# Optimization experiments

Measured on AMD Instinct MI355X. Metric: run time of the kernel, lower is better.

The kernel has to match this reference:

```python
import jax, jax.numpy as jnp
import numpy as np

N_ENT = 100000
N_REL = 500
D_IN = 128
D_OUT = 128
E_HALF = 1000000  # edges per direction; edge_index has 2*E_HALF columns
BN_EPS = 1e-5


def ccorr(a, b):
    # circular correlation: irfft(conj(rfft(a)) * rfft(b))
    d = a.shape[-1]
    return jnp.fft.irfft(jnp.conj(jnp.fft.rfft(a, axis=-1)) * jnp.fft.rfft(b, axis=-1), n=d, axis=-1)


def setup_inputs() -> dict:
    key = jax.random.key(0)
    ks = jax.random.split(key, 12)
    inv = 1.0 / np.sqrt(D_IN)
    inp = {
        "x": jax.random.normal(ks[0], (N_ENT, D_IN), dtype=jnp.float32),
        "rel_embed": jax.random.normal(ks[1], (N_REL, D_IN), dtype=jnp.float32),
        "w_in": jax.random.uniform(ks[2], (D_IN, D_OUT), minval=-inv, maxval=inv, dtype=jnp.float32),
        "w_out": jax.random.uniform(ks[3], (D_IN, D_OUT), minval=-inv, maxval=inv, dtype=jnp.float32),
        "w_loop": jax.random.uniform(ks[4], (D_IN, D_OUT), minval=-inv, maxval=inv, dtype=jnp.float32),
        "w_rel": jax.random.uniform(ks[5], (D_IN, D_OUT), minval=-inv, maxval=inv, dtype=jnp.float32),
        "loop_rel": jax.random.normal(ks[6], (1, D_IN), dtype=jnp.float32),
        "bias": jnp.zeros((D_OUT,), dtype=jnp.float32),
        "bn_weight": jnp.ones((D_OUT,), dtype=jnp.float32),
        "bn_bias": jnp.zeros((D_OUT,), dtype=jnp.float32),
        "edge_index": jax.random.randint(ks[7], (2, 2 * E_HALF), 0, N_ENT, dtype=jnp.int32),
        "edge_type": jax.random.randint(ks[8], (2 * E_HALF,), 0, N_REL, dtype=jnp.int32),
    }
    return inp


def _compute_norm(edge_index, num_ent):
    row, col = edge_index[0], edge_index[1]
    ones = jnp.ones(row.shape, dtype=jnp.float32)
    deg = jax.ops.segment_sum(ones, row, num_segments=num_ent)
    deg_inv = jnp.where(deg > 0, jax.lax.rsqrt(jnp.maximum(deg, 1.0)), 0.0)
    return deg_inv[row] * deg_inv[col]  # [E]


def _propagate(x, edge_index, edge_type, rel_all, weight, norm, num_ent):
    x_j = x[edge_index[0]]              # [E, d_in] gather source nodes
    r = rel_all[edge_type]              # [E, d_in] gather relation embeds
    m = ccorr(x_j, r) @ weight          # [E, d_out]
    if norm is not None:
        m = m * norm[:, None]
    return jax.ops.segment_sum(m, edge_index[1], num_segments=num_ent)


def reference(x, rel_embed, w_in, w_out, w_loop, w_rel, loop_rel, bias, bn_weight, bn_bias, edge_index, edge_type):
    num_ent = x.shape[0]
    rel_all = jnp.concatenate([rel_embed, loop_rel], axis=0)  # [R+1, d_in]
    e = edge_index.shape[1] // 2
    in_idx, out_idx = edge_index[:, :e], edge_index[:, e:]
    in_type, out_type = edge_type[:e], edge_type[e:]

    in_norm = _compute_norm(in_idx, num_ent)
    out_norm = _compute_norm(out_idx, num_ent)

    in_res = _propagate(x, in_idx, in_type, rel_all, w_in, in_norm, num_ent)
    out_res = _propagate(x, out_idx, out_type, rel_all, w_out, out_norm, num_ent)
    # loop edges are (i, i) with relation = last row of rel_all -> identity scatter
    loop_res = ccorr(x, rel_all[-1][None, :]) @ w_loop

    out = (in_res + out_res + loop_res) * (1.0 / 3.0) + bias
    # BatchNorm1d (training-mode batch statistics, biased variance)
    mu = jnp.mean(out, axis=0)
    var = jnp.mean((out - mu) ** 2, axis=0)
    out = (out - mu) * jax.lax.rsqrt(var + BN_EPS) * bn_weight + bn_bias

    rel_out = (rel_all @ w_rel)[:-1]
    return out, rel_out
```

## Files before the change

kernel.cpp:

```cpp
#include <hip/hip_runtime.h>
#include <cmath>

#define N_ENT 100000
#define EHALF 1000000
#define N_REL 500
#define NBUK 196
#define DPB 512
#define SCAP 7680
#define DCAP 6656
#define NSB 512
#define SPAN 1954

#ifndef M_PI
#define M_PI 3.14159265358979323846
#endif

typedef _Float16 f16x8 __attribute__((ext_vector_type(8)));
typedef _Float16 f16x4 __attribute__((ext_vector_type(4)));
typedef _Float16 f16x2 __attribute__((ext_vector_type(2)));
typedef float f32x4 __attribute__((ext_vector_type(4)));

union H16 { unsigned short u; _Float16 h; };
union HU32 { unsigned u; f16x2 h; };

__global__ void k_tabs(float* __restrict__ Ftab, float* __restrict__ Gtab,
                       _Float16* __restrict__ FtabT) {
  int i = blockIdx.x * 256 + threadIdx.x;
  if (i >= 128 * 128) return;
  int n = i >> 7, s = i & 127;
  float fv, gv;
  if (s == 0) { fv = 1.f; gv = 1.f / 384.f; }
  else if (s == 1) { float sg = (n & 1) ? -1.f : 1.f; fv = sg; gv = sg / 384.f; }
  else {
    int f = s >> 1;
    double ang = 2.0 * M_PI * (double)((f * n) & 127) / 128.0;
    if (!(s & 1)) { double c = cos(ang); fv = (float)c; gv = (float)(c * (2.0 / 384.0)); }
    else { double sv = sin(ang); fv = (float)(-sv); gv = (float)(-sv * (2.0 / 384.0)); }
  }
  Ftab[n * 128 + s] = fv;
  Gtab[s * 128 + n] = gv;
  FtabT[s * 128 + n] = (_Float16)fv;
}

__global__ void k_dftrel(const float* __restrict__ rel, const float* __restrict__ looprel,
                         const float* __restrict__ Ftab, float* __restrict__ Rf,
                         _Float16* __restrict__ RfL) {
  __shared__ float sv[128];
  int r = blockIdx.x, s = threadIdx.x;
  const float* row = (r < N_REL) ? rel + (size_t)r * 128 : looprel;
  float acc = 0.f;
  for (int n = 0; n < 128; ++n) acc += row[n] * Ftab[n * 128 + s];
  Rf[(size_t)r * 128 + s] = acc;
  sv[s] = acc;
  __syncthreads();
  if (s < 64) {
    f16x4 o;
    if (s == 0) {
      o = (f16x4){(_Float16)sv[0], (_Float16)0.f, (_Float16)0.f, (_Float16)sv[1]};
    } else {
      float rx = sv[2 * s], ry = sv[2 * s + 1];
      o = (f16x4){(_Float16)rx, (_Float16)ry, (_Float16)ry, (_Float16)(-rx)};
    }
    ((f16x4*)RfL)[(size_t)r * 64 + s] = o;
  }
}

__global__ void k_wt(const float* __restrict__ W, const float* __restrict__ Rfl,
                     _Float16* __restrict__ WT) {
  int i = blockIdx.x * 256 + threadIdx.x;
  if (i >= 384 * 128) return;
  int k = i >> 7, c = i & 127;
  float val;
  if (k < 256) {
    val = W[i];
  } else {
    int kk = k - 256;
    if (kk == 0)      val = Rfl[0] * W[i];
    else if (kk == 1) val = Rfl[1] * W[i];
    else {
      int f = kk >> 1;
      float rr = Rfl[2 * f], ri = Rfl[2 * f + 1];
      float a = W[(256 + 2 * f) * 128 + c];
      float b = W[(256 + 2 * f + 1) * 128 + c];
      val = (kk & 1) ? (ri * a - rr * b) : (rr * a + ri * b);
    }
  }
  WT[(size_t)c * 384 + k] = (_Float16)val;
}

__device__ void gemm128_body(const float* __restrict__ A, int lda,
                             const float* __restrict__ B,
                             float* __restrict__ C, int ldc,
                             int M, int K, int m0) {
  __shared__ float As[64][64];
  __shared__ float Bs[64][128];
  const int t = threadIdx.x;
  const int cg = t & 31;
  const int eg = t >> 5;
  float acc[8][4];
#pragma unroll
  for (int i = 0; i < 8; ++i)
#pragma unroll
    for (int j = 0; j < 4; ++j) acc[i][j] = 0.f;

  for (int k0 = 0; k0 < K; k0 += 64) {
#pragma unroll
    for (int p = 0; p < 4; ++p) {
      int idx = t + p * 256;
      int r = idx >> 4, c4 = idx & 15;
      int gr = m0 + r;
      float4 v = make_float4(0.f, 0.f, 0.f, 0.f);
      if (gr < M) v = *(const float4*)(A + (size_t)gr * lda + k0 + c4 * 4);
      *(float4*)&As[r][c4 * 4] = v;
    }
#pragma unroll
    for (int p = 0; p < 8; ++p) {
      int idx = t + p * 256;
      int r = idx >> 5, c4 = idx & 31;
      float4 v = *(const float4*)(B + (size_t)(k0 + r) * 128 + c4 * 4);
      *(float4*)&Bs[r][c4 * 4] = v;
    }
    __syncthreads();
#pragma unroll
    for (int k = 0; k < 64; ++k) {
      float4 bv = *(float4*)&Bs[k][cg * 4];
#pragma unroll
      for (int i = 0; i < 8; ++i) {
        float av = As[eg * 8 + i][k];
        acc[i][0] += av * bv.x; acc[i][1] += av * bv.y;
        acc[i][2] += av * bv.z; acc[i][3] += av * bv.w;
      }
    }
    __syncthreads();
  }
#pragma unroll
  for (int i = 0; i < 8; ++i) {
    int gr = m0 + eg * 8 + i;
    if (gr < M) {
      float4 v = make_float4(acc[i][0], acc[i][1], acc[i][2], acc[i][3]);
      *(float4*)(C + (size_t)gr * ldc + cg * 4) = v;
    }
  }
}

__global__ __launch_bounds__(256) void gemm128(
    const float* __restrict__ A, int lda, const float* __restrict__ B,
    float* __restrict__ C, int ldc, int M, int K) {
  gemm128_body(A, lda, B, C, ldc, M, K, blockIdx.x * 64);
}

__global__ __launch_bounds__(256) void k_wprep(
    const float* __restrict__ Gtab, const float* __restrict__ w0,
    const float* __restrict__ w1, const float* __restrict__ w2,
    float* __restrict__ Wstack) {
  int which = blockIdx.x >> 1;
  const float* B = (which == 0) ? w0 : ((which == 1) ? w1 : w2);
  gemm128_body(Gtab, 128, B, Wstack + which * 128 * 128, 128, 128, 128,
               (blockIdx.x & 1) * 64);
}

__device__ inline f16x8 loadAfrag(const _Float16* A, size_t off) {
  return *(const f16x8*)(A + off);
}
__device__ inline f16x8 loadAfrag(const float* A, size_t off) {
  float4 u = *(const float4*)(A + off);
  float4 v = *(const float4*)(A + off + 4);
  return (f16x8){(_Float16)u.x, (_Float16)u.y, (_Float16)u.z, (_Float16)u.w,
                 (_Float16)v.x, (_Float16)v.y, (_Float16)v.z, (_Float16)v.w};
}

template<int K, int KS, int MODE, typename AT>
__global__ __launch_bounds__(256) void mgemm(
    const AT* __restrict__ A, int lda,
    const _Float16* __restrict__ BT,
    _Float16* __restrict__ C, int ldc, int M,
    const float* __restrict__ bias, float* __restrict__ bnAcc) {
  __shared__ __align__(16) char lds[128 * KS * 2 + 4096];
  const int t = threadIdx.x;
  const int l = t & 63, w = t >> 6;
  const int col0 = l & 15, rg = l >> 4;
  const int rowbase = blockIdx.x * 256 + w * 64;
  const int sw = (col0 & 7) << 4;

  f32x4 acc[4][8];
  f32x4 zz = {0.f, 0.f, 0.f, 0.f};
#pragma unroll
  for (int a = 0; a < 4; ++a)
#pragma unroll
    for (int n = 0; n < 8; ++n) acc[a][n] = zz;

  for (int ks0 = 0; ks0 < K; ks0 += KS) {
    __syncthreads();
    const int CH = KS / 8;
    for (int u = t; u < 128 * CH; u += 256) {
      int col = u / CH, kc = u % CH;
      f16x8 vch = *(const f16x8*)(BT + (size_t)col * K + ks0 + kc * 8);
      *(f16x8*)(lds + col * (KS * 2) + ((kc * 16) ^ ((col & 7) << 4))) = vch;
    }
    __syncthreads();
#pragma unroll
    for (int ks = 0; ks < KS / 32; ++ks) {
      int kb = ks0 + ks * 32 + rg * 8;
      f16x8 af[4];
#pragma unroll
      for (int a = 0; a < 4; ++a) {
        int rb = rowbase + a * 16;
        if (rb < M) af[a] = loadAfrag(A, (size_t)(rb + col0) * lda + kb);
        else af[a] = (f16x8){0, 0, 0, 0, 0, 0, 0, 0};
      }
      int kc = ks * 4 + rg;
#pragma unroll
      for (int n = 0; n < 8; ++n) {
        f16x8 bf = *(const f16x8*)(lds + (n * 16 + col0) * (KS * 2) + ((kc * 16) ^ sw));
#pragma unroll
        for (int a = 0; a < 4; ++a)
          acc[a][n] = __builtin_amdgcn_mfma_f32_16x16x32_f16(af[a], bf, acc[a][n], 0, 0, 0);
      }
    }
  }

  if (MODE == 1) {
#pragma unroll
    for (int a = 0; a < 4; ++a) {
      int rb = rowbase + a * 16;
      if (rb >= M) continue;
#pragma unroll
      for (int r = 0; r < 4; ++r) {
        int row = rb + rg * 4 + r;
#pragma unroll
        for (int n = 0; n < 8; ++n) {
          int col = n * 16 + col0;
          C[(size_t)row * ldc + col] = (_Float16)acc[a][n][r];
        }
      }
    }
  } else {
    float sacc[8], qacc[8];
#pragma unroll
    for (int n = 0; n < 8; ++n) { sacc[n] = 0.f; qacc[n] = 0.f; }
#pragma unroll
    for (int a = 0; a < 4; ++a) {
      int rb = rowbase + a * 16;
      if (rb >= M) continue;
#pragma unroll
      for (int n = 0; n < 8; ++n) {
        int col = n * 16 + col0;
        float bi = bias[col];
#pragma unroll
        for (int r = 0; r < 4; ++r) {
          float val = acc[a][n][r] + bi;
          C[(size_t)(rb + rg * 4 + r) * ldc + col] = (_Float16)val;
          sacc[n] += val; qacc[n] += val * val;
        }
      }
    }
    __syncthreads();
    float* Sb = (float*)lds;
    float* Qb = Sb + 512;
#pragma unroll
    for (int n = 0; n < 8; ++n) {
      float s = sacc[n], q = qacc[n];
      s += __shfl_xor(s, 16); s += __shfl_xor(s, 32);
      q += __shfl_xor(q, 16); q += __shfl_xor(q, 32);
      if (rg == 0) { Sb[w * 128 + n * 16 + col0] = s; Qb[w * 128 + n * 16 + col0] = q; }
    }
    __syncthreads();
    if (t < 128) {
      float s = Sb[t] + Sb[128 + t] + Sb[256 + t] + Sb[384 + t];
      float q = Qb[t] + Qb[128 + t] + Qb[256 + t] + Qb[384 + t];
      atomicAdd(&bnAcc[t], s);
      atomicAdd(&bnAcc[128 + t], q);
    }
  }
}

__global__ __launch_bounds__(256) void k_split(
    const int* __restrict__ ei, const int* __restrict__ et,
    int* __restrict__ gcur,
    unsigned* __restrict__ recSI, unsigned* __restrict__ recSO,
    uint2* __restrict__ recDI, uint2* __restrict__ recDO) {
  __shared__ int bcnt[NBUK], cnt2[NBUK], base[NBUK], nn[NBUK];
  const int t = threadIdx.x;
  const int ph = blockIdx.x >> 9;
  const int blk = blockIdx.x & 511;
  const int st = blk * SPAN;
  const int en = min(st + SPAN, EHALF);

  if (t < NBUK) { bcnt[t] = 0; cnt2[t] = 0; }
  __syncthreads();

  if (ph < 2) {
    const int* key = ei + (ph ? EHALF : 0);
    int* gc = gcur + ph * NBUK;
    unsigned* rec = ph ? recSO : recSI;
    unsigned rr[8]; int bb[8];
#pragma unroll
    for (int j = 0; j < 8; ++j) {
      int e = st + j * 256 + t;
      bb[j] = -1;
      if (e < en) {
        int s = key[e];
        rr[j] = (unsigned)(s & 511) | 0x80000000u;
        bb[j] = s >> 9;
        atomicAdd(&bcnt[bb[j]], 1);
      }
    }
    __syncthreads();
    if (t < NBUK) {
      int n = bcnt[t]; nn[t] = n;
      base[t] = n ? (t * SCAP + atomicAdd(&gc[t], (n + 7) & ~7)) : 0;
    }
    __syncthreads();
#pragma unroll
    for (int j = 0; j < 8; ++j) {
      if (bb[j] >= 0) {
        int p = atomicAdd(&cnt2[bb[j]], 1);
        rec[(size_t)base[bb[j]] + p] = rr[j];
      }
    }
    __syncthreads();
    if (t < NBUK) {
      int n = nn[t];
      if (n & 7) {
        int pe = (n + 7) & ~7;
        for (int k = n; k < pe; ++k) rec[(size_t)base[t] + k] = 0u;
      }
    }
  } else {
    const int dir = ph - 2;
    const int* srcA = ei + (dir ? EHALF : 0);
    const int* dstA = ei + (dir ? 3 * EHALF : 2 * EHALF);
    const int* typA = et + (dir ? EHALF : 0);
    int* gc = gcur + (2 + dir) * NBUK;
    uint2* rec = dir ? recDO : recDI;
    unsigned w0[8], w1[8]; int bb[8];
#pragma unroll
    for (int j = 0; j < 8; ++j) {
      int e = st + j * 256 + t;
      bb[j] = -1;
      if (e < en) {
        int s = srcA[e], d = dstA[e], ty = typA[e];
        w0[j] = (unsigned)s | ((unsigned)ty << 17);
        w1[j] = (unsigned)(d & 511) | 0x80000000u;
        bb[j] = d >> 9;
        atomicAdd(&bcnt[bb[j]], 1);
      }
    }
    __syncthreads();
    if (t < NBUK) {
      int n = bcnt[t]; nn[t] = n;
      base[t] = n ? (t * DCAP + atomicAdd(&gc[t], (n + 3) & ~3)) : 0;
    }
    __syncthreads();
#pragma unroll
    for (int j = 0; j < 8; ++j) {
      if (bb[j] >= 0) {
        int p = atomicAdd(&cnt2[bb[j]], 1);
        rec[(size_t)base[bb[j]] + p] = make_uint2(w0[j], w1[j]);
      }
    }
    __syncthreads();
    if (t < NBUK) {
      int n = nn[t];
      if (n & 3) {
        int pe = (n + 3) & ~3;
        for (int k = n; k < pe; ++k) rec[(size_t)base[t] + k] = make_uint2(0u, 0u);
      }
    }
  }
}

__global__ __launch_bounds__(512) void k_dhist(
    const unsigned* __restrict__ recI, const int* __restrict__ gI,
    float* __restrict__ dinvIn,
    const unsigned* __restrict__ recO, const int* __restrict__ gO,
    float* __restrict__ dinvOut) {
  int b = blockIdx.x % NBUK;
  int dir = blockIdx.x / NBUK;
  const unsigned* rec = dir ? recO : recI;
  const int gs = b * SCAP;
  const int ge = gs + (dir ? gO : gI)[b];
  float* dinv = dir ? dinvOut : dinvIn;
  __shared__ int h[DPB];
  int t = threadIdx.x;
  h[t] = 0;
  __syncthreads();
  for (int i = gs + t; i < ge; i += 512) {
    unsigned r = rec[i];
    if (r >> 31) atomicAdd(&h[r & 511], 1);
  }
  __syncthreads();
  int ent = b * 512 + t;
  if (ent < N_ENT) {
    int d = h[t];
    dinv[ent] = (d > 0) ? rsqrtf((float)d) : 0.f;
  }
}

__global__ __launch_bounds__(512) void k_fsort(
    const uint2* __restrict__ recDI, const int* __restrict__ gDI,
    uint2* __restrict__ csrIn, int2* __restrict__ beI,
    const uint2* __restrict__ recDO, const int* __restrict__ gDO,
    uint2* __restrict__ csrOut, int2* __restrict__ beO,
    const float* __restrict__ dinvIn, const float* __restrict__ dinvOut) {
  int b = blockIdx.x % NBUK;
  int dir = blockIdx.x / NBUK;
  const uint2* rec = dir ? recDO : recDI;
  const int gs = b * DCAP;
  const int ge = gs + (dir ? gDO : gDI)[b];
  const float* dinv = dir ? dinvOut : dinvIn;
  uint2* csr = dir ? csrOut : csrIn;
  int2* be = dir ? beO : beI;
  __shared__ int h[DPB], sc[DPB], c2[DPB];
  __shared__ float dl[DPB];
  __shared__ int totv;
  int t = threadIdx.x;
  int ent = b * 512 + t;
  h[t] = 0; c2[t] = 0;
  dl[t] = (ent < N_ENT) ? dinv[ent] : 0.f;
  __syncthreads();
  for (int i = gs + t; i < ge; i += 512) {
    uint2 r = rec[i];
    if (r.y >> 31) atomicAdd(&h[r.y & 511], 1);
  }
  __syncthreads();
  sc[t] = h[t];
  __syncthreads();
  for (int o = 1; o < 512; o <<= 1) {
    int a = (t >= o) ? sc[t - o] : 0;
    __syncthreads();
    sc[t] += a;
    __syncthreads();
  }
  int excl = sc[t] - h[t];
  if (t == 511) totv = sc[511];
  if (ent < N_ENT) be[ent] = make_int2(gs + excl, gs + excl + h[t]);
  __syncthreads();
  sc[t] = excl;
  __syncthreads();
  if (t < 8) csr[(size_t)gs + totv + t] = make_uint2(0u, 0u);
  for (int i = gs + t; i < ge; i += 512) {
    uint2 r = rec[i];
    if (r.y >> 31) {
      int d = r.y & 511;
      unsigned src = r.x & 0x1FFFFu;
      float nm = dinv[src] * dl[d];
      H16 cv; cv.h = (_Float16)nm;
      int p = atomicAdd(&c2[d], 1);
      csr[(size_t)gs + sc[d] + p] =
          make_uint2((src * 3u) << 8,
                     (r.x >> 17) | ((unsigned)cv.u << 16));
    }
  }
}

__device__ inline float dot2f(f16x2 a, f16x2 b, float c) {
#if __has_builtin(__builtin_amdgcn_fdot2)
  return __builtin_amdgcn_fdot2(a, b, c, false);
#else
  return fmaf((float)a[0], (float)b[0], fmaf((float)a[1], (float)b[1], c));
#endif
}

__device__ inline void b4load(const uint2* __restrict__ csr, int base,
                              const char* __restrict__ Xb, const char* __restrict__ Rb,
                              unsigned lxc, unsigned lr,
                              uint2 q[4], f16x2 xv[4], f16x4 rv[4]) {
// ... 48 lines not shown
  while (nbi > 0) {
    uint2 qa[4]; f16x2 xa[4]; f16x4 ra[4];
    b4load(csrIn, i, Xb, Rb, lxc, lr, qa, xa, ra);
    b4math(qa, i, ie, xa, ra, aix, aiy);
    i += 4; --nbi;
  }
  while (nbo > 0) {
    uint2 qb[4]; f16x2 xb[4]; f16x4 rb[4];
    b4load(csrOut, o, Xb, Rb, lxc, lr, qb, xb, rb);
    b4math(qb, o, oe, xb, rb, aox, aoy);
    o += 4; --nbo;
  }

  *(f16x2*)((char*)Abuf + (size_t)v * 768 + 4u * l) = (f16x2){(_Float16)aix, (_Float16)aiy};
  *(f16x2*)((char*)Abuf + (size_t)v * 768 + 256 + 4u * l) = (f16x2){(_Float16)aox, (_Float16)aoy};
}

__global__ void k_norm(const _Float16* __restrict__ tmp, float* __restrict__ out,
                       const float* __restrict__ bnAcc, const float* __restrict__ bnw,
                       const float* __restrict__ bnb) {
  __shared__ float ss[256];
  int t = threadIdx.x;
  if (t < 128) {
    float mu = bnAcc[t] * (1.f / (float)N_ENT);
    float var = bnAcc[128 + t] * (1.f / (float)N_ENT) - mu * mu;
    float sc = bnw[t] * rsqrtf(var + 1e-5f);
    ss[t] = sc; ss[128 + t] = bnb[t] - mu * sc;
  }
  __syncthreads();
  int i = blockIdx.x * 256 + t;
  f16x8 v = ((const f16x8*)tmp)[i];
  int cb = (i & 15) * 8;
  float4 o0, o1;
  o0.x = (float)v[0] * ss[cb]     + ss[128 + cb];
  o0.y = (float)v[1] * ss[cb + 1] + ss[129 + cb];
  o0.z = (float)v[2] * ss[cb + 2] + ss[130 + cb];
  o0.w = (float)v[3] * ss[cb + 3] + ss[131 + cb];
  o1.x = (float)v[4] * ss[cb + 4] + ss[132 + cb];
  o1.y = (float)v[5] * ss[cb + 5] + ss[133 + cb];
  o1.z = (float)v[6] * ss[cb + 6] + ss[134 + cb];
  o1.w = (float)v[7] * ss[cb + 7] + ss[135 + cb];
  ((float4*)out)[2 * i] = o0;
  ((float4*)out)[2 * i + 1] = o1;
}

extern "C" void kernel_launch(void* const* d_in, const int* in_sizes, int n_in,
                              void* d_out, int out_size, void* d_ws, size_t ws_size,
                              hipStream_t stream) {
  const float* x       = (const float*)d_in[0];
  const float* rel     = (const float*)d_in[1];
  const float* w_in    = (const float*)d_in[2];
  const float* w_out   = (const float*)d_in[3];
  const float* w_loop  = (const float*)d_in[4];
  const float* w_rel   = (const float*)d_in[5];
  const float* looprel = (const float*)d_in[6];
  const float* bias    = (const float*)d_in[7];
  const float* bnw     = (const float*)d_in[8];
  const float* bnb     = (const float*)d_in[9];
// ... 19 lines not shown
  float* dinvIn   = (float*)alloc(N_ENT * 4);
  float* dinvOut  = (float*)alloc(N_ENT * 4);
  int*   gcur     = (int*)alloc(4 * NBUK * 4);
  int2*  beI      = (int2*)alloc((size_t)N_ENT * 8);
  int2*  beO      = (int2*)alloc((size_t)N_ENT * 8);
  unsigned* recSI = (unsigned*)alloc((size_t)NBUK * SCAP * 4);
  unsigned* recSO = (unsigned*)alloc((size_t)NBUK * SCAP * 4);
  uint2* recDI    = (uint2*)alloc((size_t)NBUK * DCAP * 8);
  uint2* recDO    = (uint2*)alloc((size_t)NBUK * DCAP * 8);
  uint2* csrIn    = (uint2*)alloc((size_t)NBUK * DCAP * 8);
  uint2* csrOut   = (uint2*)alloc((size_t)NBUK * DCAP * 8);
  float* bnAcc    = (float*)alloc(256 * 4);

  int* gSI = gcur;
  int* gSO = gcur + NBUK;

  hipMemsetAsync(gcur, 0, 4 * NBUK * 4, stream);
  hipMemsetAsync(bnAcc, 0, 256 * 4, stream);

  k_tabs<<<64, 256, 0, stream>>>(Ftab, Gtab, FtabT);
  k_dftrel<<<501, 128, 0, stream>>>(rel, looprel, Ftab, Rf, RfL);
  k_wprep<<<6, 256, 0, stream>>>(Gtab, w_in, w_out, w_loop, Wstack);
  k_wt<<<192, 256, 0, stream>>>(Wstack, Rf + 500 * 128, WT);

  mgemm<128, 128, 1, float><<<(N_ENT + 255) / 256, 256, 0, stream>>>(
      x, 128, FtabT, Abuf + 256, 384, N_ENT, nullptr, nullptr);

  k_split<<<4 * NSB, 256, 0, stream>>>(ei, et, gcur, recSI, recSO, recDI, recDO);
  k_dhist<<<2 * NBUK, 512, 0, stream>>>(recSI, gSI, dinvIn, recSO, gSO, dinvOut);
  k_fsort<<<2 * NBUK, 512, 0, stream>>>(recDI, gcur + 2 * NBUK, csrIn, beI,
                                        recDO, gcur + 3 * NBUK, csrOut, beO,
                                        dinvIn, dinvOut);

  k_agg<<<N_ENT / 4, 256, 0, stream>>>(Abuf, RfL, csrIn, beI, csrOut, beO);

  mgemm<384, 192, 2, _Float16><<<(N_ENT + 255) / 256, 256, 0, stream>>>(
      Abuf, 384, WT, tmpC, 128, N_ENT, bias, bnAcc);
  k_norm<<<(N_ENT * 128 / 8) / 256, 256, 0, stream>>>(tmpC, out, bnAcc, bnw, bnb);

  gemm128<<<(N_REL + 63) / 64, 256, 0, stream>>>(rel, 128, w_rel, out + (size_t)N_ENT * 128, 128, N_REL, 128);
}
```

Baseline: 309.8 us.

## Fuse independent small kernels into combined launches to cut launch count

Merges independent stages into multi-role kernels that dispatch on block index. The x DFT GEMM, edge split and relation DFT share one launch, weight prep shares one with degree histogram, and the weight transpose shares one with the CSR sort. The relation GEMM shares a launch with the final normalization. The two memsets move into the table-building kernel. This cuts launch count and serialization gaps between small kernels. The cost is shared LDS sized for the largest role and larger per-launch register footprints, which may lower occupancy for some roles.

```diff
diff --git a/kernel.cpp b/kernel.cpp
--- a/kernel.cpp
+++ b/kernel.cpp
@@ -10,6 +10,7 @@
 #define DCAP 6656
 #define NSB 512
 #define SPAN 1954
+#define XFB 391
 
 #ifndef M_PI
 #define M_PI 3.14159265358979323846
@@ -24,7 +25,12 @@
 union HU32 { unsigned u; f16x2 h; };
 
 __global__ void k_tabs(float* __restrict__ Ftab, float* __restrict__ Gtab,
-                       _Float16* __restrict__ FtabT) {
+                       _Float16* __restrict__ FtabT,
+                       int* __restrict__ gcur, float* __restrict__ bnAcc) {
+  if (blockIdx.x == 0) {
+    for (int j = threadIdx.x; j < 4 * NBUK; j += 256) gcur[j] = 0;
+    bnAcc[threadIdx.x] = 0.f;
+  }
   int i = blockIdx.x * 256 + threadIdx.x;
   if (i >= 128 * 128) return;
   int n = i >> 7, s = i & 127;
@@ -42,32 +48,396 @@
   FtabT[s * 128 + n] = (_Float16)fv;
 }
 
-__global__ void k_dftrel(const float* __restrict__ rel, const float* __restrict__ looprel,
-                         const float* __restrict__ Ftab, float* __restrict__ Rf,
-                         _Float16* __restrict__ RfL) {
-  __shared__ float sv[128];
-  int r = blockIdx.x, s = threadIdx.x;
-  const float* row = (r < N_REL) ? rel + (size_t)r * 128 : looprel;
-  float acc = 0.f;
-  for (int n = 0; n < 128; ++n) acc += row[n] * Ftab[n * 128 + s];
-  Rf[(size_t)r * 128 + s] = acc;
-  sv[s] = acc;
-  __syncthreads();
-  if (s < 64) {
+__device__ void gemm128_body(char* smem, const float* __restrict__ A, int lda,
+                             const float* __restrict__ B,
+                             float* __restrict__ C, int ldc,
+                             int M, int K, int m0) {
+  float (*As)[64] = (float(*)[64])smem;
+  float (*Bs)[128] = (float(*)[128])(smem + 64 * 64 * 4);
+  const int t = threadIdx.x;
+  const int cg = t & 31;
+  const int eg = t >> 5;
+  float acc[8][4];
+#pragma unroll
+  for (int i = 0; i < 8; ++i)
+#pragma unroll
+    for (int j = 0; j < 4; ++j) acc[i][j] = 0.f;
+
+  for (int k0 = 0; k0 < K; k0 += 64) {
+#pragma unroll
+    for (int p = 0; p < 4; ++p) {
+      int idx = t + p * 256;
+      int r = idx >> 4, c4 = idx & 15;
+      int gr = m0 + r;
+      float4 v = make_float4(0.f, 0.f, 0.f, 0.f);
+      if (gr < M) v = *(const float4*)(A + (size_t)gr * lda + k0 + c4 * 4);
+      *(float4*)&As[r][c4 * 4] = v;
+    }
+#pragma unroll
+    for (int p = 0; p < 8; ++p) {
+      int idx = t + p * 256;
+      int r = idx >> 5, c4 = idx & 31;
+      float4 v = *(const float4*)(B + (size_t)(k0 + r) * 128 + c4 * 4);
+      *(float4*)&Bs[r][c4 * 4] = v;
+    }
+    __syncthreads();
+#pragma unroll
+    for (int k = 0; k < 64; ++k) {
+      float4 bv = *(float4*)&Bs[k][cg * 4];
+#pragma unroll
+      for (int i = 0; i < 8; ++i) {
+        float av = As[eg * 8 + i][k];
+        acc[i][0] += av * bv.x; acc[i][1] += av * bv.y;
+        acc[i][2] += av * bv.z; acc[i][3] += av * bv.w;
+      }
+    }
+    __syncthreads();
+  }
+#pragma unroll
+  for (int i = 0; i < 8; ++i) {
+    int gr = m0 + eg * 8 + i;
+    if (gr < M) {
+      float4 v = make_float4(acc[i][0], acc[i][1], acc[i][2], acc[i][3]);
+      *(float4*)(C + (size_t)gr * ldc + cg * 4) = v;
+    }
+  }
+}
+
+__device__ inline f16x8 loadAfrag(const _Float16* A, size_t off) {
+  return *(const f16x8*)(A + off);
+}
+__device__ inline f16x8 loadAfrag(const float* A, size_t off) {
+  float4 u = *(const float4*)(A + off);
+  float4 v = *(const float4*)(A + off + 4);
+  return (f16x8){(_Float16)u.x, (_Float16)u.y, (_Float16)u.z, (_Float16)u.w,
+                 (_Float16)v.x, (_Float16)v.y, (_Float16)v.z, (_Float16)v.w};
+}
+
+template<int K, int KS, int MODE, typename AT>
+__device__ void mgemm_body(char* lds, int bid,
+                           const AT* __restrict__ A, int lda,
+                           const _Float16* __restrict__ BT,
+                           _Float16* __restrict__ C, int ldc, int M,
+                           const float* __restrict__ bias, float* __restrict__ bnAcc) {
+  const int t = threadIdx.x;
+  const int l = t & 63, w = t >> 6;
+  const int col0 = l & 15, rg = l >> 4;
+  const int rowbase = bid * 256 + w * 64;
+  const int sw = (col0 & 7) << 4;
+
+  f32x4 acc[4][8];
+  f32x4 zz = {0.f, 0.f, 0.f, 0.f};
+#pragma unroll
+  for (int a = 0; a < 4; ++a)
+#pragma unroll
+    for (int n = 0; n < 8; ++n) acc[a][n] = zz;
+
+  for (int ks0 = 0; ks0 < K; ks0 += KS) {
+    __syncthreads();
+    const int CH = KS / 8;
+    for (int u = t; u < 128 * CH; u += 256) {
+      int col = u / CH, kc = u % CH;
+      f16x8 vch = *(const f16x8*)(BT + (size_t)col * K + ks0 + kc * 8);
+      *(f16x8*)(lds + col * (KS * 2) + ((kc * 16) ^ ((col & 7) << 4))) = vch;
+    }
+    __syncthreads();
+#pragma unroll
+    for (int ks = 0; ks < KS / 32; ++ks) {
+      int kb = ks0 + ks * 32 + rg * 8;
+      f16x8 af[4];
+#pragma unroll
+      for (int a = 0; a < 4; ++a) {
+        int rb = rowbase + a * 16;
+        if (rb < M) af[a] = loadAfrag(A, (size_t)(rb + col0) * lda + kb);
+        else af[a] = (f16x8){0, 0, 0, 0, 0, 0, 0, 0};
+      }
+      int kc = ks * 4 + rg;
+#pragma unroll
+      for (int n = 0; n < 8; ++n) {
+        f16x8 bf = *(const f16x8*)(lds + (n * 16 + col0) * (KS * 2) + ((kc * 16) ^ sw));
+#pragma unroll
+        for (int a = 0; a < 4; ++a)
+          acc[a][n] = __builtin_amdgcn_mfma_f32_16x16x32_f16(af[a], bf, acc[a][n], 0, 0, 0);
+      }
+    }
+  }
+
+  if (MODE == 1) {
+#pragma unroll
+    for (int a = 0; a < 4; ++a) {
+      int rb = rowbase + a * 16;
+      if (rb >= M) continue;
+#pragma unroll
+      for (int r = 0; r < 4; ++r) {
+        int row = rb + rg * 4 + r;
+#pragma unroll
+        for (int n = 0; n < 8; ++n) {
+          int col = n * 16 + col0;
+          C[(size_t)row * ldc + col] = (_Float16)acc[a][n][r];
+        }
+      }
+    }
+  } else {
+    float sacc[8], qacc[8];
+#pragma unroll
+    for (int n = 0; n < 8; ++n) { sacc[n] = 0.f; qacc[n] = 0.f; }
+#pragma unroll
+    for (int a = 0; a < 4; ++a) {
+      int rb = rowbase + a * 16;
+      if (rb >= M) continue;
+#pragma unroll
+      for (int n = 0; n < 8; ++n) {
+        int col = n * 16 + col0;
+        float bi = bias[col];
+#pragma unroll
+        for (int r = 0; r < 4; ++r) {
+          float val = acc[a][n][r] + bi;
+          C[(size_t)(rb + rg * 4 + r) * ldc + col] = (_Float16)val;
+          sacc[n] += val; qacc[n] += val * val;
+        }
+      }
+    }
+    __syncthreads();
+    float* Sb = (float*)lds;
+    float* Qb = Sb + 512;
+#pragma unroll
+    for (int n = 0; n < 8; ++n) {
+      float s = sacc[n], q = qacc[n];
+      s += __shfl_xor(s, 16); s += __shfl_xor(s, 32);
+      q += __shfl_xor(q, 16); q += __shfl_xor(q, 32);
+      if (rg == 0) { Sb[w * 128 + n * 16 + col0] = s; Qb[w * 128 + n * 16 + col0] = q; }
+    }
+    __syncthreads();
+    if (t < 128) {
+      float s = Sb[t] + Sb[128 + t] + Sb[256 + t] + Sb[384 + t];
+      float q = Qb[t] + Qb[128 + t] + Qb[256 + t] + Qb[384 + t];
+      atomicAdd(&bnAcc[t], s);
+      atomicAdd(&bnAcc[128 + t], q);
+    }
+  }
+}
+
+__device__ void split_body(char* smem, int bid,
+                           const int* __restrict__ ei, const int* __restrict__ et,
+                           int* __restrict__ gcur,
+                           unsigned* __restrict__ recSI, unsigned* __restrict__ recSO,
+                           uint2* __restrict__ recDI, uint2* __restrict__ recDO) {
+  int* bcnt = (int*)smem;
+  int* cnt2 = bcnt + NBUK;
+  int* base = cnt2 + NBUK;
+  int* nn   = base + NBUK;
+  const int t = threadIdx.x;
+  const int ph = bid >> 9;
+  const int blk = bid & 511;
+  const int st = blk * SPAN;
+  const int en = min(st + SPAN, EHALF);
+
+  if (t < NBUK) { bcnt[t] = 0; cnt2[t] = 0; }
+  __syncthreads();
+
+  if (ph < 2) {
+    const int* key = ei + (ph ? EHALF : 0);
+    int* gc = gcur + ph * NBUK;
+    unsigned* rec = ph ? recSO : recSI;
+    unsigned rr[8]; int bb[8];
+#pragma unroll
+    for (int j = 0; j < 8; ++j) {
+      int e = st + j * 256 + t;
+      bb[j] = -1;
+      if (e < en) {
+        int s = key[e];
+        rr[j] = (unsigned)(s & 511) | 0x80000000u;
+        bb[j] = s >> 9;
+        atomicAdd(&bcnt[bb[j]], 1);
+      }
+    }
+    __syncthreads();
+    if (t < NBUK) {
+      int n = bcnt[t]; nn[t] = n;
+      base[t] = n ? (t * SCAP + atomicAdd(&gc[t], (n + 7) & ~7)) : 0;
+    }
+    __syncthreads();
+#pragma unroll
+    for (int j = 0; j < 8; ++j) {
+      if (bb[j] >= 0) {
+        int p = atomicAdd(&cnt2[bb[j]], 1);
+        rec[(size_t)base[bb[j]] + p] = rr[j];
+      }
+    }
+    __syncthreads();
+    if (t < NBUK) {
+      int n = nn[t];
+      if (n & 7) {
+        int pe = (n + 7) & ~7;
+        for (int k = n; k < pe; ++k) rec[(size_t)base[t] + k] = 0u;
+      }
+    }
+  } else {
+    const int dir = ph - 2;
+    const int* srcA = ei + (dir ? EHALF : 0);
+    const int* dstA = ei + (dir ? 3 * EHALF : 2 * EHALF);
+    const int* typA = et + (dir ? EHALF : 0);
+    int* gc = gcur + (2 + dir) * NBUK;
+    uint2* rec = dir ? recDO : recDI;
+    unsigned w0[8], w1[8]; int bb[8];
+#pragma unroll
+    for (int j = 0; j < 8; ++j) {
+      int e = st + j * 256 + t;
+      bb[j] = -1;
+      if (e < en) {
+        int s = srcA[e], d = dstA[e], ty = typA[e];
+        w0[j] = (unsigned)s | ((unsigned)ty << 17);
+        w1[j] = (unsigned)(d & 511) | 0x80000000u;
+        bb[j] = d >> 9;
+        atomicAdd(&bcnt[bb[j]], 1);
+      }
+    }
+    __syncthreads();
+    if (t < NBUK) {
+      int n = bcnt[t]; nn[t] = n;
+      base[t] = n ? (t * DCAP + atomicAdd(&gc[t], (n + 3) & ~3)) : 0;
+    }
+    __syncthreads();
+#pragma unroll
+    for (int j = 0; j < 8; ++j) {
+      if (bb[j] >= 0) {
+        int p = atomicAdd(&cnt2[bb[j]], 1);
+        rec[(size_t)base[bb[j]] + p] = make_uint2(w0[j], w1[j]);
+      }
+    }
+    __syncthreads();
+    if (t < NBUK) {
+      int n = nn[t];
+      if (n & 3) {
+        int pe = (n + 3) & ~3;
+        for (int k = n; k < pe; ++k) rec[(size_t)base[t] + k] = make_uint2(0u, 0u);
+      }
+    }
+  }
+}
+
+__device__ void dftrel_body(char* smem, int blk,
+                            const float* __restrict__ rel, const float* __restrict__ looprel,
+                            const float* __restrict__ Ftab, float* __restrict__ Rf,
+                            _Float16* __restrict__ RfL) {
+  float* sv = (float*)smem;
+  int t = threadIdx.x;
+  int r = blk * 2 + (t >> 7);
+  int s = t & 127;
+  if (r < 501) {
+    const float* row = (r < N_REL) ? rel + (size_t)r * 128 : looprel;
+    float acc = 0.f;
+    for (int n = 0; n < 128; ++n) acc += row[n] * Ftab[n * 128 + s];
+    Rf[(size_t)r * 128 + s] = acc;
+    sv[t] = acc;
+  }
+  __syncthreads();
+  if (r < 501 && s < 64) {
+    int bse = t & 128;
     f16x4 o;
     if (s == 0) {
-      o = (f16x4){(_Float16)sv[0], (_Float16)0.f, (_Float16)0.f, (_Float16)sv[1]};
+      o = (f16x4){(_Float16)sv[bse], (_Float16)0.f, (_Float16)0.f, (_Float16)sv[bse + 1]};
     } else {
-      float rx = sv[2 * s], ry = sv[2 * s + 1];
+      float rx = sv[bse + 2 * s], ry = sv[bse + 2 * s + 1];
       o = (f16x4){(_Float16)rx, (_Float16)ry, (_Float16)ry, (_Float16)(-rx)};
     }
     ((f16x4*)RfL)[(size_t)r * 64 + s] = o;
   }
 }
 
-__global__ void k_wt(const float* __restrict__ W, const float* __restrict__ Rfl,
-                     _Float16* __restrict__ WT) {
-  int i = blockIdx.x * 256 + threadIdx.x;
+__device__ void dhist_body(char* smem, int bid,
+                           const unsigned* __restrict__ recI, const int* __restrict__ gI,
+                           float* __restrict__ dinvIn,
+                           const unsigned* __restrict__ recO, const int* __restrict__ gO,
+                           float* __restrict__ dinvOut) {
+  int b = bid % NBUK;
+  int dir = bid / NBUK;
+  const unsigned* rec = dir ? recO : recI;
+  const int gs = b * SCAP;
+  const int ge = gs + (dir ? gO : gI)[b];
+  float* dinv = dir ? dinvOut : dinvIn;
+  int* h = (int*)smem;
+  int t = threadIdx.x;
+  h[t] = 0; h[t + 256] = 0;
+  __syncthreads();
+  for (int i = gs + t; i < ge; i += 256) {
+    unsigned r = rec[i];
+    if (r >> 31) atomicAdd(&h[r & 511], 1);
+  }
+  __syncthreads();
+#pragma unroll
+  for (int j = 0; j < 2; ++j) {
+    int bin = t + j * 256;
+    int ent = b * 512 + bin;
+    if (ent < N_ENT) {
+      int d = h[bin];
+      dinv[ent] = (d > 0) ? rsqrtf((float)d) : 0.f;
+    }
+  }
+}
+
+__device__ void fsort_body(char* smem, int bid,
+                           const uint2* __restrict__ recDI, const int* __restrict__ gDI,
+                           uint2* __restrict__ csrIn, int2* __restrict__ beI,
+                           const uint2* __restrict__ recDO, const int* __restrict__ gDO,
+                           uint2* __restrict__ csrOut, int2* __restrict__ beO,
+                           const float* __restrict__ dinvIn, const float* __restrict__ dinvOut) {
+  int b = bid % NBUK;
+  int dir = bid / NBUK;
+  const uint2* rec = dir ? recDO : recDI;
+  const int gs = b * DCAP;
+  const int ge = gs + (dir ? gDO : gDI)[b];
+  const float* dinv = dir ? dinvOut : dinvIn;
+  uint2* csr = dir ? csrOut : csrIn;
+  int2* be = dir ? beO : beI;
+  int* h  = (int*)smem;
+  int* sc = h + 512;
+  int* c2 = sc + 512;
+  float* dl = (float*)(c2 + 512);
+  int* totv = (int*)(dl + 512);
+  int t = threadIdx.x;
+  int ent = b * 512 + t;
+  h[t] = 0; c2[t] = 0;
+  dl[t] = (ent < N_ENT) ? dinv[ent] : 0.f;
+  __syncthreads();
+  for (int i = gs + t; i < ge; i += 512) {
+    uint2 r = rec[i];
+    if (r.y >> 31) atomicAdd(&h[r.y & 511], 1);
+  }
+  __syncthreads();
+  sc[t] = h[t];
+  __syncthreads();
+  for (int o = 1; o < 512; o <<= 1) {
+    int a = (t >= o) ? sc[t - o] : 0;
+    __syncthreads();
+    sc[t] += a;
+    __syncthreads();
+  }
+  int excl = sc[t] - h[t];
+  if (t == 511) *totv = sc[511];
+  if (ent < N_ENT) be[ent] = make_int2(gs + excl, gs + excl + h[t]);
+  __syncthreads();
+  sc[t] = excl;
+  __syncthreads();
+  if (t < 8) csr[(size_t)gs + *totv + t] = make_uint2(0u, 0u);
+  for (int i = gs + t; i < ge; i += 512) {
+    uint2 r = rec[i];
+    if (r.y >> 31) {
+      int d = r.y & 511;
+      unsigned src = r.x & 0x1FFFFu;
+      float nm = dinv[src] * dl[d];
+      H16 cv; cv.h = (_Float16)nm;
+      int p = atomicAdd(&c2[d], 1);
+      csr[(size_t)gs + sc[d] + p] =
+          make_uint2((src * 3u) << 8,
+                     (r.x >> 17) | ((unsigned)cv.u << 16));
+    }
+  }
+}
+
+__device__ void wt_body(int wb, const float* __restrict__ W, const float* __restrict__ Rfl,
+                        _Float16* __restrict__ WT) {
+  int i = wb * 512 + threadIdx.x;
   if (i >= 384 * 128) return;
   int k = i >> 7, c = i & 127;
   float val;
@@ -88,369 +458,103 @@
   WT[(size_t)c * 384 + k] = (_Float16)val;
 }
 
-__device__ void gemm128_body(const float* __restrict__ A, int lda,
-                             const float* __restrict__ B,
-                             float* __restrict__ C, int ldc,
-                             int M, int K, int m0) {
-  __shared__ float As[64][64];
-  __shared__ float Bs[64][128];
-  const int t = threadIdx.x;
-  const int cg = t & 31;
-  const int eg = t >> 5;
-  float acc[8][4];
-#pragma unroll
-  for (int i = 0; i < 8; ++i)
-#pragma unroll
-    for (int j = 0; j < 4; ++j) acc[i][j] = 0.f;
-
-  for (int k0 = 0; k0 < K; k0 += 64) {
-#pragma unroll
-    for (int p = 0; p < 4; ++p) {
-      int idx = t + p * 256;
-      int r = idx >> 4, c4 = idx & 15;
-      int gr = m0 + r;
-      float4 v = make_float4(0.f, 0.f, 0.f, 0.f);
-      if (gr < M) v = *(const float4*)(A + (size_t)gr * lda + k0 + c4 * 4);
-      *(float4*)&As[r][c4 * 4] = v;
-    }
-#pragma unroll
-    for (int p = 0; p < 8; ++p) {
-      int idx = t + p * 256;
-      int r = idx >> 5, c4 = idx & 31;
-      float4 v = *(const float4*)(B + (size_t)(k0 + r) * 128 + c4 * 4);
-      *(float4*)&Bs[r][c4 * 4] = v;
-    }
-    __syncthreads();
-#pragma unroll
-    for (int k = 0; k < 64; ++k) {
-      float4 bv = *(float4*)&Bs[k][cg * 4];
-#pragma unroll
-      for (int i = 0; i < 8; ++i) {
-        float av = As[eg * 8 + i][k];
-        acc[i][0] += av * bv.x; acc[i][1] += av * bv.y;
-        acc[i][2] += av * bv.z; acc[i][3] += av * bv.w;
-      }
-    }
-    __syncthreads();
-  }
-#pragma unroll
-  for (int i = 0; i < 8; ++i) {
-    int gr = m0 + eg * 8 + i;
-    if (gr < M) {
-      float4 v = make_float4(acc[i][0], acc[i][1], acc[i][2], acc[i][3]);
-      *(float4*)(C + (size_t)gr * ldc + cg * 4) = v;
-    }
-  }
-}
-
-__global__ __launch_bounds__(256) void gemm128(
-    const float* __restrict__ A, int lda, const float* __restrict__ B,
-    float* __restrict__ C, int ldc, int M, int K) {
-  gemm128_body(A, lda, B, C, ldc, M, K, blockIdx.x * 64);
-}
-
-__global__ __launch_bounds__(256) void k_wprep(
+__device__ void norm_body(char* smem, int bid, const _Float16* __restrict__ tmp,
+                          float* __restrict__ out, const float* __restrict__ bnAcc,
+                          const float* __restrict__ bnw, const float* __restrict__ bnb) {
+  float* ss = (float*)smem;
+  int t = threadIdx.x;
+  if (t < 128) {
+    float mu = bnAcc[t] * (1.f / (float)N_ENT);
+    float var = bnAcc[128 + t] * (1.f / (float)N_ENT) - mu * mu;
+    float sc = bnw[t] * rsqrtf(var + 1e-5f);
+    ss[t] = sc; ss[128 + t] = bnb[t] - mu * sc;
+  }
+  __syncthreads();
+  int i = bid * 256 + t;
+  f16x8 v = ((const f16x8*)tmp)[i];
+  int cb = (i & 15) * 8;
+  float4 o0, o1;
+  o0.x = (float)v[0] * ss[cb]     + ss[128 + cb];
+  o0.y = (float)v[1] * ss[cb + 1] + ss[129 + cb];
+  o0.z = (float)v[2] * ss[cb + 2] + ss[130 + cb];
+  o0.w = (float)v[3] * ss[cb + 3] + ss[131 + cb];
+  o1.x = (float)v[4] * ss[cb + 4] + ss[132 + cb];
+  o1.y = (float)v[5] * ss[cb + 5] + ss[133 + cb];
+  o1.z = (float)v[6] * ss[cb + 6] + ss[134 + cb];
+  o1.w = (float)v[7] * ss[cb + 7] + ss[135 + cb];
+  ((float4*)out)[2 * i] = o0;
+  ((float4*)out)[2 * i + 1] = o1;
+}
+
+__global__ __launch_bounds__(256) void k_front(
+    const float* __restrict__ x, const _Float16* __restrict__ FtabT, _Float16* __restrict__ Abuf,
+    const int* __restrict__ ei, const int* __restrict__ et, int* __restrict__ gcur,
+    unsigned* __restrict__ recSI, unsigned* __restrict__ recSO,
+    uint2* __restrict__ recDI, uint2* __restrict__ recDO,
+    const float* __restrict__ rel, const float* __restrict__ looprel,
+    const float* __restrict__ Ftab, float* __restrict__ Rf, _Float16* __restrict__ RfL) {
+  __shared__ __align__(16) char smem[37120];
+  int b = blockIdx.x;
+  if (b < XFB) {
+    mgemm_body<128, 128, 1, float>(smem, b, x, 128, FtabT, Abuf + 256, 384, N_ENT,
+                                   nullptr, nullptr);
+  } else if (b < XFB + 4 * NSB) {
+    split_body(smem, b - XFB, ei, et, gcur, recSI, recSO, recDI, recDO);
+  } else {
+    dftrel_body(smem, b - XFB - 4 * NSB, rel, looprel, Ftab, Rf, RfL);
+  }
+}
+
+__global__ __launch_bounds__(256) void k_mid1(
     const float* __restrict__ Gtab, const float* __restrict__ w0,
-    const float* __restrict__ w1, const float* __restrict__ w2,
-    float* __restrict__ Wstack) {
-  int which = blockIdx.x >> 1;
-  const float* B = (which == 0) ? w0 : ((which == 1) ? w1 : w2);
-  gemm128_body(Gtab, 128, B, Wstack + which * 128 * 128, 128, 128, 128,
-               (blockIdx.x & 1) * 64);
-}
-
-__device__ inline f16x8 loadAfrag(const _Float16* A, size_t off) {
-  return *(const f16x8*)(A + off);
-}
-__device__ inline f16x8 loadAfrag(const float* A, size_t off) {
-  float4 u = *(const float4*)(A + off);
-  float4 v = *(const float4*)(A + off + 4);
-  return (f16x8){(_Float16)u.x, (_Float16)u.y, (_Float16)u.z, (_Float16)u.w,
-                 (_Float16)v.x, (_Float16)v.y, (_Float16)v.z, (_Float16)v.w};
-}
-
-template<int K, int KS, int MODE, typename AT>
-__global__ __launch_bounds__(256) void mgemm(
-    const AT* __restrict__ A, int lda,
-    const _Float16* __restrict__ BT,
-    _Float16* __restrict__ C, int ldc, int M,
-    const float* __restrict__ bias, float* __restrict__ bnAcc) {
-  __shared__ __align__(16) char lds[128 * KS * 2 + 4096];
-  const int t = threadIdx.x;
-  const int l = t & 63, w = t >> 6;
-  const int col0 = l & 15, rg = l >> 4;
-  const int rowbase = blockIdx.x * 256 + w * 64;
-  const int sw = (col0 & 7) << 4;
-
-  f32x4 acc[4][8];
-  f32x4 zz = {0.f, 0.f, 0.f, 0.f};
-#pragma unroll
-  for (int a = 0; a < 4; ++a)
-#pragma unroll
-    for (int n = 0; n < 8; ++n) acc[a][n] = zz;
-
-  for (int ks0 = 0; ks0 < K; ks0 += KS) {
-    __syncthreads();
-    const int CH = KS / 8;
-    for (int u = t; u < 128 * CH; u += 256) {
-      int col = u / CH, kc = u % CH;
-      f16x8 vch = *(const f16x8*)(BT + (size_t)col * K + ks0 + kc * 8);
-      *(f16x8*)(lds + col * (KS * 2) + ((kc * 16) ^ ((col & 7) << 4))) = vch;
-    }
-    __syncthreads();
-#pragma unroll
-    for (int ks = 0; ks < KS / 32; ++ks) {
-      int kb = ks0 + ks * 32 + rg * 8;
-      f16x8 af[4];
-#pragma unroll
-      for (int a = 0; a < 4; ++a) {
-        int rb = rowbase + a * 16;
-        if (rb < M) af[a] = loadAfrag(A, (size_t)(rb + col0) * lda + kb);
-        else af[a] = (f16x8){0, 0, 0, 0, 0, 0, 0, 0};
-      }
-      int kc = ks * 4 + rg;
-#pragma unroll
-      for (int n = 0; n < 8; ++n) {
-        f16x8 bf = *(const f16x8*)(lds + (n * 16 + col0) * (KS * 2) + ((kc * 16) ^ sw));
-#pragma unroll
-        for (int a = 0; a < 4; ++a)
-          acc[a][n] = __builtin_amdgcn_mfma_f32_16x16x32_f16(af[a], bf, acc[a][n], 0, 0, 0);
-      }
-    }
-  }
-
-  if (MODE == 1) {
-#pragma unroll
-    for (int a = 0; a < 4; ++a) {
-      int rb = rowbase + a * 16;
-      if (rb >= M) continue;
-#pragma unroll
-      for (int r = 0; r < 4; ++r) {
-        int row = rb + rg * 4 + r;
-#pragma unroll
-        for (int n = 0; n < 8; ++n) {
-          int col = n * 16 + col0;
-          C[(size_t)row * ldc + col] = (_Float16)acc[a][n][r];
-        }
-      }
-    }
+    const float* __restrict__ w1, const float* __restrict__ w2, float* __restrict__ Wstack,
+    const unsigned* __restrict__ recSI, const int* __restrict__ gSI, float* __restrict__ dinvIn,
+    const unsigned* __restrict__ recSO, const int* __restrict__ gSO, float* __restrict__ dinvOut) {
+  __shared__ __align__(16) char smem[49280];
+  int b = blockIdx.x;
+  if (b < 6) {
+    int which = b >> 1;
+    const float* B = (which == 0) ? w0 : ((which == 1) ? w1 : w2);
+    gemm128_body(smem, Gtab, 128, B, Wstack + which * 128 * 128, 128, 128, 128, (b & 1) * 64);
   } else {
-    float sacc[8], qacc[8];
-#pragma unroll
-    for (int n = 0; n < 8; ++n) { sacc[n] = 0.f; qacc[n] = 0.f; }
-#pragma unroll
-    for (int a = 0; a < 4; ++a) {
-      int rb = rowbase + a * 16;
-      if (rb >= M) continue;
-#pragma unroll
-      for (int n = 0; n < 8; ++n) {
-        int col = n * 16 + col0;
-        float bi = bias[col];
-#pragma unroll
-        for (int r = 0; r < 4; ++r) {
-          float val = acc[a][n][r] + bi;
-          C[(size_t)(rb + rg * 4 + r) * ldc + col] = (_Float16)val;
-          sacc[n] += val; qacc[n] += val * val;
-        }
-      }
-    }
-    __syncthreads();
-    float* Sb = (float*)lds;
-    float* Qb = Sb + 512;
-#pragma unroll
-    for (int n = 0; n < 8; ++n) {
-      float s = sacc[n], q = qacc[n];
-      s += __shfl_xor(s, 16); s += __shfl_xor(s, 32);
-      q += __shfl_xor(q, 16); q += __shfl_xor(q, 32);
-      if (rg == 0) { Sb[w * 128 + n * 16 + col0] = s; Qb[w * 128 + n * 16 + col0] = q; }
-    }
-    __syncthreads();
-    if (t < 128) {
-      float s = Sb[t] + Sb[128 + t] + Sb[256 + t] + Sb[384 + t];
-      float q = Qb[t] + Qb[128 + t] + Qb[256 + t] + Qb[384 + t];
-      atomicAdd(&bnAcc[t], s);
-      atomicAdd(&bnAcc[128 + t], q);
-    }
-  }
-}
-
-__global__ __launch_bounds__(256) void k_split(
-    const int* __restrict__ ei, const int* __restrict__ et,
-    int* __restrict__ gcur,
-    unsigned* __restrict__ recSI, unsigned* __restrict__ recSO,
-    uint2* __restrict__ recDI, uint2* __restrict__ recDO) {
-  __shared__ int bcnt[NBUK], cnt2[NBUK], base[NBUK], nn[NBUK];
-  const int t = threadIdx.x;
-  const int ph = blockIdx.x >> 9;
-  const int blk = blockIdx.x & 511;
-  const int st = blk * SPAN;
-  const int en = min(st + SPAN, EHALF);
-
-  if (t < NBUK) { bcnt[t] = 0; cnt2[t] = 0; }
-  __syncthreads();
-
-  if (ph < 2) {
-    const int* key = ei + (ph ? EHALF : 0);
-    int* gc = gcur + ph * NBUK;
-    unsigned* rec = ph ? recSO : recSI;
-    unsigned rr[8]; int bb[8];
-#pragma unroll
-    for (int j = 0; j < 8; ++j) {
-      int e = st + j * 256 + t;
-      bb[j] = -1;
-      if (e < en) {
-        int s = key[e];
-        rr[j] = (unsigned)(s & 511) | 0x80000000u;
-        bb[j] = s >> 9;
-        atomicAdd(&bcnt[bb[j]], 1);
-      }
-    }
-    __syncthreads();
-    if (t < NBUK) {
-      int n = bcnt[t]; nn[t] = n;
-      base[t] = n ? (t * SCAP + atomicAdd(&gc[t], (n + 7) & ~7)) : 0;
-    }
-    __syncthreads();
-#pragma unroll
-    for (int j = 0; j < 8; ++j) {
-      if (bb[j] >= 0) {
-        int p = atomicAdd(&cnt2[bb[j]], 1);
-        rec[(size_t)base[bb[j]] + p] = rr[j];
-      }
-    }
-    __syncthreads();
-    if (t < NBUK) {
-      int n = nn[t];
-      if (n & 7) {
-        int pe = (n + 7) & ~7;
-        for (int k = n; k < pe; ++k) rec[(size_t)base[t] + k] = 0u;
-      }
-    }
-  } else {
-    const int dir = ph - 2;
-    const int* srcA = ei + (dir ? EHALF : 0);
-    const int* dstA = ei + (dir ? 3 * EHALF : 2 * EHALF);
-    const int* typA = et + (dir ? EHALF : 0);
-    int* gc = gcur + (2 + dir) * NBUK;
-    uint2* rec = dir ? recDO : recDI;
-    unsigned w0[8], w1[8]; int bb[8];
-#pragma unroll
-    for (int j = 0; j < 8; ++j) {
-      int e = st + j * 256 + t;
-      bb[j] = -1;
-      if (e < en) {
-        int s = srcA[e], d = dstA[e], ty = typA[e];
-        w0[j] = (unsigned)s | ((unsigned)ty << 17);
-        w1[j] = (unsigned)(d & 511) | 0x80000000u;
-        bb[j] = d >> 9;
-        atomicAdd(&bcnt[bb[j]], 1);
-      }
-    }
-    __syncthreads();
-    if (t < NBUK) {
-      int n = bcnt[t]; nn[t] = n;
-      base[t] = n ? (t * DCAP + atomicAdd(&gc[t], (n + 3) & ~3)) : 0;
-    }
-    __syncthreads();
-#pragma unroll
-    for (int j = 0; j < 8; ++j) {
-      if (bb[j] >= 0) {
-        int p = atomicAdd(&cnt2[bb[j]], 1);
-        rec[(size_t)base[bb[j]] + p] = make_uint2(w0[j], w1[j]);
-      }
-    }
-    __syncthreads();
-    if (t < NBUK) {
-      int n = nn[t];
-      if (n & 3) {
-        int pe = (n + 3) & ~3;
-        for (int k = n; k < pe; ++k) rec[(size_t)base[t] + k] = make_uint2(0u, 0u);
-      }
-    }
-  }
-}
-
-__global__ __launch_bounds__(512) void k_dhist(
-    const unsigned* __restrict__ recI, const int* __restrict__ gI,
-    float* __restrict__ dinvIn,
-    const unsigned* __restrict__ recO, const int* __restrict__ gO,
-    float* __restrict__ dinvOut) {
-  int b = blockIdx.x % NBUK;
-  int dir = blockIdx.x / NBUK;
-  const unsigned* rec = dir ? recO : recI;
-  const int gs = b * SCAP;
-  const int ge = gs + (dir ? gO : gI)[b];
-  float* dinv = dir ? dinvOut : dinvIn;
-  __shared__ int h[DPB];
-  int t = threadIdx.x;
-  h[t] = 0;
-  __syncthreads();
-  for (int i = gs + t; i < ge; i += 512) {
-    unsigned r = rec[i];
-    if (r >> 31) atomicAdd(&h[r & 511], 1);
-  }
-  __syncthreads();
-  int ent = b * 512 + t;
-  if (ent < N_ENT) {
-    int d = h[t];
-    dinv[ent] = (d > 0) ? rsqrtf((float)d) : 0.f;
-  }
-}
-
-__global__ __launch_bounds__(512) void k_fsort(
+    dhist_body(smem, b - 6, recSI, gSI, dinvIn, recSO, gSO, dinvOut);
+  }
+}
+
+__global__ __launch_bounds__(512) void k_mid2(
     const uint2* __restrict__ recDI, const int* __restrict__ gDI,
     uint2* __restrict__ csrIn, int2* __restrict__ beI,
     const uint2* __restrict__ recDO, const int* __restrict__ gDO,
     uint2* __restrict__ csrOut, int2* __restrict__ beO,
-    const float* __restrict__ dinvIn, const float* __restrict__ dinvOut) {
-  int b = blockIdx.x % NBUK;
-  int dir = blockIdx.x / NBUK;
-  const uint2* rec = dir ? recDO : recDI;
-  const int gs = b * DCAP;
-  const int ge = gs + (dir ? gDO : gDI)[b];
-  const float* dinv = dir ? dinvOut : dinvIn;
-  uint2* csr = dir ? csrOut : csrIn;
-  int2* be = dir ? beO : beI;
-  __shared__ int h[DPB], sc[DPB], c2[DPB];
-  __shared__ float dl[DPB];
-  __shared__ int totv;
-  int t = threadIdx.x;
-  int ent = b * 512 + t;
-  h[t] = 0; c2[t] = 0;
-  dl[t] = (ent < N_ENT) ? dinv[ent] : 0.f;
-  __syncthreads();
-  for (int i = gs + t; i < ge; i += 512) {
-    uint2 r = rec[i];
-    if (r.y >> 31) atomicAdd(&h[r.y & 511], 1);
-  }
-  __syncthreads();
-  sc[t] = h[t];
-  __syncthreads();
-  for (int o = 1; o < 512; o <<= 1) {
-    int a = (t >= o) ? sc[t - o] : 0;
-    __syncthreads();
-    sc[t] += a;
-    __syncthreads();
-  }
-  int excl = sc[t] - h[t];
-  if (t == 511) totv = sc[511];
-  if (ent < N_ENT) be[ent] = make_int2(gs + excl, gs + excl + h[t]);
-  __syncthreads();
-  sc[t] = excl;
-  __syncthreads();
-  if (t < 8) csr[(size_t)gs + totv + t] = make_uint2(0u, 0u);
-  for (int i = gs + t; i < ge; i += 512) {
-    uint2 r = rec[i];
-    if (r.y >> 31) {
-      int d = r.y & 511;
-      unsigned src = r.x & 0x1FFFFu;
-      float nm = dinv[src] * dl[d];
-      H16 cv; cv.h = (_Float16)nm;
-      int p = atomicAdd(&c2[d], 1);
-      csr[(size_t)gs + sc[d] + p] =
-          make_uint2((src * 3u) << 8,
-                     (r.x >> 17) | ((unsigned)cv.u << 16));
-    }
+    const float* __restrict__ dinvIn, const float* __restrict__ dinvOut,
+    const float* __restrict__ Wstack, const float* __restrict__ Rfl, _Float16* __restrict__ WT) {
+  __shared__ __align__(16) char smem[8448];
+  int b = blockIdx.x;
+  if (b < 2 * NBUK) {
+    fsort_body(smem, b, recDI, gDI, csrIn, beI, recDO, gDO, csrOut, beO, dinvIn, dinvOut);
+  } else {
+    wt_body(b - 2 * NBUK, Wstack, Rfl, WT);
+  }
+}
+
+__global__ __launch_bounds__(256) void k_mgemm384(
+    const _Float16* __restrict__ A, const _Float16* __restrict__ BT,
+    _Float16* __restrict__ C, int M,
+    const float* __restrict__ bias, float* __restrict__ bnAcc) {
+  __shared__ __align__(16) char lds[53504];
+  mgemm_body<384, 192, 2, _Float16>(lds, blockIdx.x, A, 384, BT, C, 128, M, bias, bnAcc);
+}
+
+__global__ __launch_bounds__(256) void k_back(
+    const float* __restrict__ rel, const float* __restrict__ w_rel, float* __restrict__ out,
+    const _Float16* __restrict__ tmp, const float* __restrict__ bnAcc,
+    const float* __restrict__ bnw, const float* __restrict__ bnb) {
+  __shared__ __align__(16) char smem[49280];
+  int b = blockIdx.x;
+  if (b < 8) {
+    gemm128_body(smem, rel, 128, w_rel, out + (size_t)N_ENT * 128, 128, N_REL, 128, b * 64);
+  } else {
+    norm_body(smem, b - 8, tmp, out, bnAcc, bnw, bnb);
   }
 }
 
@@ -529,34 +633,6 @@
 
   *(f16x2*)((char*)Abuf + (size_t)v * 768 + 4u * l) = (f16x2){(_Float16)aix, (_Float16)aiy};
   *(f16x2*)((char*)Abuf + (size_t)v * 768 + 256 + 4u * l) = (f16x2){(_Float16)aox, (_Float16)aoy};
-}
-
-__global__ void k_norm(const _Float16* __restrict__ tmp, float* __restrict__ out,
-                       const float* __restrict__ bnAcc, const float* __restrict__ bnw,
-                       const float* __restrict__ bnb) {
-  __shared__ float ss[256];
-  int t = threadIdx.x;
-  if (t < 128) {
-    float mu = bnAcc[t] * (1.f / (float)N_ENT);
-    float var = bnAcc[128 + t] * (1.f / (float)N_ENT) - mu * mu;
-    float sc = bnw[t] * rsqrtf(var + 1e-5f);
-    ss[t] = sc; ss[128 + t] = bnb[t] - mu * sc;
-  }
-  __syncthreads();
-  int i = blockIdx.x * 256 + t;
-  f16x8 v = ((const f16x8*)tmp)[i];
-  int cb = (i & 15) * 8;
-  float4 o0, o1;
-  o0.x = (float)v[0] * ss[cb]     + ss[128 + cb];
-  o0.y = (float)v[1] * ss[cb + 1] + ss[129 + cb];
-  o0.z = (float)v[2] * ss[cb + 2] + ss[130 + cb];
-  o0.w = (float)v[3] * ss[cb + 3] + ss[131 + cb];
-  o1.x = (float)v[4] * ss[cb + 4] + ss[132 + cb];
-  o1.y = (float)v[5] * ss[cb + 5] + ss[133 + cb];
-  o1.z = (float)v[6] * ss[cb + 6] + ss[134 + cb];
-  o1.w = (float)v[7] * ss[cb + 7] + ss[135 + cb];
-  ((float4*)out)[2 * i] = o0;
-  ((float4*)out)[2 * i + 1] = o1;
 }
 
 extern "C" void kernel_launch(void* const* d_in, const int* in_sizes, int n_in,
@@ -606,29 +682,26 @@
 
   int* gSI = gcur;
   int* gSO = gcur + NBUK;
-
-  hipMemsetAsync(gcur, 0, 4 * NBUK * 4, stream);
-  hipMemsetAsync(bnAcc, 0, 256 * 4, stream);
-
-  k_tabs<<<64, 256, 0, stream>>>(Ftab, Gtab, FtabT);
-  k_dftrel<<<501, 128, 0, stream>>>(rel, looprel, Ftab, Rf, RfL);
-  k_wprep<<<6, 256, 0, stream>>>(Gtab, w_in, w_out, w_loop, Wstack);
-  k_wt<<<192, 256, 0, stream>>>(Wstack, Rf + 500 * 128, WT);
-
-  mgemm<128, 128, 1, float><<<(N_ENT + 255) / 256, 256, 0, stream>>>(
-      x, 128, FtabT, Abuf + 256, 384, N_ENT, nullptr, nullptr);
-
-  k_split<<<4 * NSB, 256, 0, stream>>>(ei, et, gcur, recSI, recSO, recDI, recDO);
-  k_dhist<<<2 * NBUK, 512, 0, stream>>>(recSI, gSI, dinvIn, recSO, gSO, dinvOut);
-  k_fsort<<<2 * NBUK, 512, 0, stream>>>(recDI, gcur + 2 * NBUK, csrIn, beI,
-                                        recDO, gcur + 3 * NBUK, csrOut, beO,
-                                        dinvIn, dinvOut);
+  int* gDI = gcur + 2 * NBUK;
+  int* gDO = gcur + 3 * NBUK;
+
+  k_tabs<<<64, 256, 0, stream>>>(Ftab, Gtab, FtabT, gcur, bnAcc);
+
+  k_front<<<XFB + 4 * NSB + 251, 256, 0, stream>>>(
+      x, FtabT, Abuf, ei, et, gcur, recSI, recSO, recDI, recDO,
+      rel, looprel, Ftab, Rf, RfL);
+
+  k_mid1<<<6 + 2 * NBUK, 256, 0, stream>>>(
+      Gtab, w_in, w_out, w_loop, Wstack, recSI, gSI, dinvIn, recSO, gSO, dinvOut);
+
+  k_mid2<<<2 * NBUK + 96, 512, 0, stream>>>(
+      recDI, gDI, csrIn, beI, recDO, gDO, csrOut, beO, dinvIn, dinvOut,
+      Wstack, Rf + 500 * 128, WT);
 
   k_agg<<<N_ENT / 4, 256, 0, stream>>>(Abuf, RfL, csrIn, beI, csrOut, beO);
 
-  mgemm<384, 192, 2, _Float16><<<(N_ENT + 255) / 256, 256, 0, stream>>>(
-      Abuf, 384, WT, tmpC, 128, N_ENT, bias, bnAcc);
-  k_norm<<<(N_ENT * 128 / 8) / 256, 256, 0, stream>>>(tmpC, out, bnAcc, bnw, bnb);
-
-  gemm128<<<(N_REL + 63) / 64, 256, 0, stream>>>(rel, 128, w_rel, out + (size_t)N_ENT * 128, 128, N_REL, 128);
-}
+  k_mgemm384<<<XFB, 256, 0, stream>>>(Abuf, WT, tmpC, N_ENT, bias, bnAcc);
+
+  k_back<<<8 + (N_ENT * 128 / 8) / 256, 256, 0, stream>>>(
+      rel, w_rel, out, tmpC, bnAcc, bnw, bnb);
+}
```

Result: slower. 328.5 us (+6.0%).
